# Kernel optimization log

Measured on AMD Instinct MI355X. Metric: run time of the kernel, lower is better.

The kernel has to match this reference:

```python
import jax, jax.numpy as jnp
import numpy as np

N_NODES = 100000
N_EDGES = 1600000
IN_DIM = 128
OUT_DIM = 64
SLOPE = 0.2


def setup_inputs() -> dict:
    key = jax.random.key(0)
    k1, k2, k3, k4 = jax.random.split(key, 4)
    h = jax.random.normal(k1, (N_NODES, IN_DIM), dtype=jnp.float32)
    W = jax.random.normal(k2, (OUT_DIM, IN_DIM), dtype=jnp.float32) * (1.0 / np.sqrt(IN_DIM))
    src = jax.random.randint(k3, (N_EDGES,), 0, N_NODES, dtype=jnp.int64)
    dst = jax.random.randint(k4, (N_EDGES,), 0, N_NODES, dtype=jnp.int64)
    return {"h": h, "W": W, "src": src, "dst": dst}


def reference(h, W, src, dst):
    n = h.shape[0]
    z = h @ W.T                                   # [N, out_dim]
    z_src = z[src]                                # [E, out_dim]
    z_dst = z[dst]                                # [E, out_dim]
    e = jax.nn.leaky_relu(jnp.sum(z_src * z_dst, axis=1), negative_slope=SLOPE)  # [E]
    # segment softmax over incoming edges of each destination node
    m = jax.ops.segment_max(e, dst, num_segments=n)        # [N], -inf for isolated nodes
    ex = jnp.exp(e - m[dst])                                # [E]
    denom = jax.ops.segment_sum(ex, dst, num_segments=n)    # [N]
    alpha = ex / denom[dst]                                 # [E]
    agg = jax.ops.segment_sum(alpha[:, None] * z_src, dst, num_segments=n)  # [N, out_dim]
    return jax.nn.elu(agg)
```

## Files before the change

kernel.cpp:

```cpp
#include <hip/hip_runtime.h>
#include <math.h>

#define SLOPE 0.2f
#define LOG2E 1.4426950408889634f

__global__ __launch_bounds__(256, 8) void gemm_hist_kernel(const float* __restrict__ h,
                                                           const float* __restrict__ W,
                                                           float* __restrict__ z,
                                                           const int* __restrict__ dst,
                                                           int* __restrict__ cnt,
                                                           int* __restrict__ rank,
                                                           int n, int ne, int nbGemm) {
    if ((int)blockIdx.x >= nbGemm) {
        int i = (blockIdx.x - nbGemm) * 256 + threadIdx.x;
        int base = i * 4;
        if (base + 3 < ne) {
            int4 d = *(const int4*)(dst + base);
            int4 r;
            r.x = atomicAdd(&cnt[d.x], 1);
            r.y = atomicAdd(&cnt[d.y], 1);
            r.z = atomicAdd(&cnt[d.z], 1);
            r.w = atomicAdd(&cnt[d.w], 1);
            *(int4*)(rank + base) = r;
        } else if (base < ne) {
            for (int rr = base; rr < ne; rr++) rank[rr] = atomicAdd(&cnt[dst[rr]], 1);
        }
        return;
    }

    __shared__ float ws[128][36];
    int t = threadIdx.x;
    int nblk = blockIdx.x >> 1;
    int ch0  = (blockIdx.x & 1) << 5;
    const float4* __restrict__ W4 = reinterpret_cast<const float4*>(W);
#pragma unroll
    for (int j = 0; j < 4; j++) {
        int idx = t + j * 256;
        int o  = idx >> 5;
        int kq = idx & 31;
        float4 w = W4[(size_t)(ch0 + o) * 32 + kq];
        int k = kq << 2;
        int col = o ^ ((kq & 7) << 2);
        ws[k + 0][col] = w.x; ws[k + 1][col] = w.y;
        ws[k + 2][col] = w.z; ws[k + 3][col] = w.w;
    }
    __syncthreads();

    int ng = t >> 3, og = t & 7;
    int n0 = nblk * 64 + ng * 2;
    if (n0 >= n) return;
    const float* __restrict__ hp = h + (size_t)n0 * 128;

    float acc[2][4] = {};
#pragma unroll 4
    for (int k = 0; k < 128; k += 4) {
        int m = (k >> 2) & 7;
        int colb = (og ^ m) << 2;
        float4 hv[2], wv[4];
#pragma unroll
        for (int i = 0; i < 2; i++) hv[i] = *(const float4*)(hp + i * 128 + k);
#pragma unroll
        for (int kk = 0; kk < 4; kk++) wv[kk] = *(const float4*)&ws[k + kk][colb];
#pragma unroll
        for (int i = 0; i < 2; i++) {
            acc[i][0] += hv[i].x * wv[0].x + hv[i].y * wv[1].x + hv[i].z * wv[2].x + hv[i].w * wv[3].x;
            acc[i][1] += hv[i].x * wv[0].y + hv[i].y * wv[1].y + hv[i].z * wv[2].y + hv[i].w * wv[3].y;
            acc[i][2] += hv[i].x * wv[0].z + hv[i].y * wv[1].z + hv[i].z * wv[2].z + hv[i].w * wv[3].z;
            acc[i][3] += hv[i].x * wv[0].w + hv[i].y * wv[1].w + hv[i].z * wv[2].w + hv[i].w * wv[3].w;
        }
    }
#pragma unroll
    for (int i = 0; i < 2; i++) {
        *(float4*)&z[(size_t)(n0 + i) * 64 + ch0 + og * 4] =
            make_float4(acc[i][0], acc[i][1], acc[i][2], acc[i][3]);
    }
}

__global__ __launch_bounds__(256) void scan1(const int* __restrict__ cnt,
                                             int* __restrict__ starts,
                                             int* __restrict__ bsums, int n) {
    __shared__ int ls[256];
    int tbase = blockIdx.x * 4096 + threadIdx.x * 16;
    int v[16];
    int s = 0;
#pragma unroll
    for (int k = 0; k < 16; k++) {
        int idx = tbase + k;
        int c = idx < n ? cnt[idx] : 0;
        v[k] = c; s += c;
    }
    ls[threadIdx.x] = s;
    __syncthreads();
    for (int off = 1; off < 256; off <<= 1) {
        int t = threadIdx.x >= off ? ls[threadIdx.x - off] : 0;
        __syncthreads();
        ls[threadIdx.x] += t;
        __syncthreads();
    }
    int run = ls[threadIdx.x] - s;
    if (threadIdx.x == 255) bsums[blockIdx.x] = ls[255];
#pragma unroll
    for (int k = 0; k < 16; k++) {
        int idx = tbase + k;
        if (idx < n) starts[idx] = run;
        run += v[k];
    }
}

__global__ __launch_bounds__(256) void scan3(int* __restrict__ starts,
                                             const int* __restrict__ bsums,
                                             int n, int ne) {
    __shared__ int base_s;
    int i = blockIdx.x * 256 + threadIdx.x;
    if (threadIdx.x == 0) {
        int reg = (int)(blockIdx.x >> 4);
        int s = 0;
        for (int b = 0; b < reg; b++) s += bsums[b];
        base_s = s;
        if (blockIdx.x == 0) starts[n] = ne;
    }
    __syncthreads();
    if (i < n) starts[i] += base_s;
}

__global__ __launch_bounds__(256) void scatter8_kernel(const int* __restrict__ src,
                                                       const int* __restrict__ dst,
                                                       const int* __restrict__ starts,
                                                       const int* __restrict__ rank,
                                                       int* __restrict__ csr_src, int ne) {
    int i = blockIdx.x * 256 + threadIdx.x;
    int base = i * 8;
    if (base + 7 < ne) {
        int4 s0 = *(const int4*)(src + base),  s1 = *(const int4*)(src + base + 4);
        int4 d0 = *(const int4*)(dst + base),  d1 = *(const int4*)(dst + base + 4);
        int4 r0 = *(const int4*)(rank + base), r1 = *(const int4*)(rank + base + 4);
        csr_src[starts[d0.x] + r0.x] = s0.x;
        csr_src[starts[d0.y] + r0.y] = s0.y;
        csr_src[starts[d0.z] + r0.z] = s0.z;
        csr_src[starts[d0.w] + r0.w] = s0.w;
        csr_src[starts[d1.x] + r1.x] = s1.x;
        csr_src[starts[d1.y] + r1.y] = s1.y;
        csr_src[starts[d1.z] + r1.z] = s1.z;
        csr_src[starts[d1.w] + r1.w] = s1.w;
    } else {
        for (int r = base; r < ne; r++)
            csr_src[starts[dst[r]] + rank[r]] = src[r];
    }
}

__global__ __launch_bounds__(256) void fused_node(const float4* __restrict__ z4,
                                                  const int* __restrict__ starts,
                                                  const int* __restrict__ csr_src,
                                                  float4* __restrict__ out4, int n) {
    int node = blockIdx.x * 4 + (threadIdx.x >> 6);
    if (node >= n) return;
    int lane = threadIdx.x & 63;
    int g = lane >> 4;
    int q = lane & 15;
    int rs = starts[node], re = starts[node + 1];
    float4 zd = z4[(size_t)node * 16 + q];

    float m2 = -1e30f, denom = 0.f;
    float4 acc = make_float4(0.f, 0.f, 0.f, 0.f);

    for (int c = rs; c < re; c += 64) {
        int j = c + lane;
        int sv = j < re ? csr_src[j] : 0;
        int cn = min(64, re - c);
        bool val0 = g < cn;
        int  s0 = __shfl(sv, val0 ? g : 0);
        float4 v0 = z4[(size_t)s0 * 16 + q];
        bool val1 = 4 + g < cn;
        int  s1 = __shfl(sv, val1 ? 4 + g : 0);
        float4 v1 = z4[(size_t)s1 * 16 + q];
        for (int k = 0; k < cn; k += 4) {
            int idx2 = k + 8 + g;
            bool val2 = idx2 < cn;
            int  s2 = __shfl(sv, val2 ? idx2 : 0);
            float4 v2 = z4[(size_t)s2 * 16 + q];
            float p = v0.x * zd.x + v0.y * zd.y + v0.z * zd.z + v0.w * zd.w;
#pragma unroll
            for (int msk = 1; msk < 16; msk <<= 1) p += __shfl_xor(p, msk);
            float e = p > 0.f ? p : SLOPE * p;
            float e2 = e * LOG2E;
            e2 = val0 ? e2 : -2e30f;
            if (__any(e2 > m2)) {
                float mnew = fmaxf(m2, e2);
                float sc = exp2f(m2 - mnew);
                float ex = exp2f(e2 - mnew);
                denom = fmaf(denom, sc, ex);
                acc.x = fmaf(acc.x, sc, ex * v0.x);
                acc.y = fmaf(acc.y, sc, ex * v0.y);
                acc.z = fmaf(acc.z, sc, ex * v0.z);
                acc.w = fmaf(acc.w, sc, ex * v0.w);
                m2 = mnew;
            } else {
                float ex = exp2f(e2 - m2);
                denom += ex;
                acc.x = fmaf(ex, v0.x, acc.x);
                acc.y = fmaf(ex, v0.y, acc.y);
                acc.z = fmaf(ex, v0.z, acc.z);
                acc.w = fmaf(ex, v0.w, acc.w);
            }
            v0 = v1; val0 = val1;
            v1 = v2; val1 = val2;
        }
    }
#pragma unroll
    for (int msk = 16; msk < 64; msk <<= 1) {
        float mo  = __shfl_xor(m2, msk);
        float dno = __shfl_xor(denom, msk);
        float ax = __shfl_xor(acc.x, msk);
        float ay = __shfl_xor(acc.y, msk);
        float az = __shfl_xor(acc.z, msk);
        float aw = __shfl_xor(acc.w, msk);
        float mnew = fmaxf(m2, mo);
        float ss = exp2f(m2 - mnew), so = exp2f(mo - mnew);
        denom = fmaf(denom, ss, dno * so);
        acc.x = fmaf(acc.x, ss, ax * so);
        acc.y = fmaf(acc.y, ss, ay * so);
        acc.z = fmaf(acc.z, ss, az * so);
        acc.w = fmaf(acc.w, ss, aw * so);
        m2 = mnew;
    }
    if (lane < 16) {
        float inv = denom > 0.f ? 1.f / denom : 0.f;
        float4 r; float x;
        x = acc.x * inv; r.x = x > 0.f ? x : __expf(x) - 1.f;
        x = acc.y * inv; r.y = x > 0.f ? x : __expf(x) - 1.f;
        x = acc.z * inv; r.z = x > 0.f ? x : __expf(x) - 1.f;
        x = acc.w * inv; r.w = x > 0.f ? x : __expf(x) - 1.f;
        out4[(size_t)node * 16 + q] = r;
    }
}

extern "C" void kernel_launch(void* const* d_in, const int* in_sizes, int n_in,
                              void* d_out, int out_size, void* d_ws, size_t ws_size,
                              hipStream_t stream) {
    const float* h   = (const float*)d_in[0];
    const float* W   = (const float*)d_in[1];
    const int*   src = (const int*)d_in[2];
    const int*   dst = (const int*)d_in[3];
    int n  = in_sizes[0] / 128;
    int ne = in_sizes[2];

    float* z       = (float*)d_ws;
    int*   rank    = (int*)(z + (size_t)n * 64);
    int*   csr_src = rank + ne;
    int*   cnt     = csr_src + ne;
    int*   starts  = cnt + n;
    int*   bsums   = starts + ((n + 5) & ~3);

    int nbGemm = ((n + 63) / 64) * 2;
    int nbHist = (ne / 4 + 255) / 256;
    int nb_scan = (n + 4095) / 4096;

    hipMemsetAsync(cnt, 0, (size_t)n * sizeof(int), stream);
    gemm_hist_kernel<<<nbGemm + nbHist, 256, 0, stream>>>(h, W, z, dst, cnt, rank,
                                                          n, ne, nbGemm);
    scan1<<<nb_scan, 256, 0, stream>>>(cnt, starts, bsums, n);
    scan3<<<(n + 255) / 256, 256, 0, stream>>>(starts, bsums, n, ne);
    scatter8_kernel<<<(ne / 8 + 255) / 256, 256, 0, stream>>>(src, dst, starts,
                                                              rank, csr_src, ne);
    fused_node<<<(n + 3) / 4, 256, 0, stream>>>((const float4*)z, starts, csr_src,
                                                (float4*)d_out, n);
}
```

Measured before the change: 207.0 us.

## Privatize histogram into 8 counter copies, pack ranks as 16-bit, interleave GEMM/hist blocks

The destination histogram is split across 8 private counter arrays, chosen by edge chunk, to spread atomic traffic. The scan sums the 8 copies, and scan3 turns each copy into its own exclusive offset base so the scatter can index it directly. Per-edge ranks are stored as 16-bit values to halve that traffic. Histogram blocks are also interleaved 1:2 with GEMM blocks so both kinds of work run together. The cost is 8x larger counter memset and scan reads, plus an implicit assumption that the histogram and GEMM block counts line up and that per-copy ranks fit in 16 bits.

```diff
diff --git a/kernel.cpp b/kernel.cpp
--- a/kernel.cpp
+++ b/kernel.cpp
@@ -8,30 +8,37 @@
                                                            const float* __restrict__ W,
                                                            float* __restrict__ z,
                                                            const int* __restrict__ dst,
-                                                           int* __restrict__ cnt,
-                                                           int* __restrict__ rank,
-                                                           int n, int ne, int nbGemm) {
-    if ((int)blockIdx.x >= nbGemm) {
-        int i = (blockIdx.x - nbGemm) * 256 + threadIdx.x;
+                                                           int* __restrict__ cnt8,
+                                                           unsigned short* __restrict__ rank,
+                                                           int n, int ne) {
+    int g = blockIdx.x / 3;
+    int r = blockIdx.x % 3;
+    if (r == 2) {
+        int* __restrict__ cnt = cnt8 + (size_t)(g & 7) * n;
+        int i = g * 256 + threadIdx.x;
         int base = i * 4;
         if (base + 3 < ne) {
             int4 d = *(const int4*)(dst + base);
-            int4 r;
-            r.x = atomicAdd(&cnt[d.x], 1);
-            r.y = atomicAdd(&cnt[d.y], 1);
-            r.z = atomicAdd(&cnt[d.z], 1);
-            r.w = atomicAdd(&cnt[d.w], 1);
-            *(int4*)(rank + base) = r;
+            unsigned int r0 = atomicAdd(&cnt[d.x], 1);
+            unsigned int r1 = atomicAdd(&cnt[d.y], 1);
+            unsigned int r2 = atomicAdd(&cnt[d.z], 1);
+            unsigned int r3 = atomicAdd(&cnt[d.w], 1);
+            uint2 packed;
+            packed.x = (r1 << 16) | (r0 & 0xFFFF);
+            packed.y = (r3 << 16) | (r2 & 0xFFFF);
+            *(uint2*)(rank + base) = packed;
         } else if (base < ne) {
-            for (int rr = base; rr < ne; rr++) rank[rr] = atomicAdd(&cnt[dst[rr]], 1);
+            for (int rr = base; rr < ne; rr++)
+                rank[rr] = (unsigned short)atomicAdd(&cnt[dst[rr]], 1);
         }
         return;
     }
 
     __shared__ float ws[128][36];
     int t = threadIdx.x;
-    int nblk = blockIdx.x >> 1;
-    int ch0  = (blockIdx.x & 1) << 5;
+    int gemmIdx = 2 * g + r;
+    int nblk = gemmIdx >> 1;
+    int ch0  = (gemmIdx & 1) << 5;
     const float4* __restrict__ W4 = reinterpret_cast<const float4*>(W);
 #pragma unroll
     for (int j = 0; j < 4; j++) {
@@ -76,19 +83,35 @@
     }
 }
 
-__global__ __launch_bounds__(256) void scan1(const int* __restrict__ cnt,
+__global__ __launch_bounds__(256) void scan1(const int* __restrict__ cnt8,
                                              int* __restrict__ starts,
                                              int* __restrict__ bsums, int n) {
     __shared__ int ls[256];
     int tbase = blockIdx.x * 4096 + threadIdx.x * 16;
-    int v[16];
+    int tot[16];
+#pragma unroll
+    for (int k = 0; k < 16; k++) tot[k] = 0;
+    if (tbase + 15 < n) {
+#pragma unroll
+        for (int c = 0; c < 8; c++) {
+            const int* cp = cnt8 + (size_t)c * n + tbase;
+#pragma unroll
+            for (int q = 0; q < 4; q++) {
+                int4 v = *(const int4*)(cp + q * 4);
+                tot[q * 4 + 0] += v.x; tot[q * 4 + 1] += v.y;
+                tot[q * 4 + 2] += v.z; tot[q * 4 + 3] += v.w;
+            }
+        }
+    } else {
+        for (int k = 0; k < 16; k++) {
+            int idx = tbase + k;
+            if (idx < n)
+                for (int c = 0; c < 8; c++) tot[k] += cnt8[(size_t)c * n + idx];
+        }
+    }
     int s = 0;
 #pragma unroll
-    for (int k = 0; k < 16; k++) {
-        int idx = tbase + k;
-        int c = idx < n ? cnt[idx] : 0;
-        v[k] = c; s += c;
-    }
+    for (int k = 0; k < 16; k++) s += tot[k];
     ls[threadIdx.x] = s;
     __syncthreads();
     for (int off = 1; off < 256; off <<= 1) {
@@ -103,12 +126,13 @@
     for (int k = 0; k < 16; k++) {
         int idx = tbase + k;
         if (idx < n) starts[idx] = run;
-        run += v[k];
+        run += tot[k];
     }
 }
 
 __global__ __launch_bounds__(256) void scan3(int* __restrict__ starts,
                                              const int* __restrict__ bsums,
+                                             int* __restrict__ cnt8,
                                              int n, int ne) {
     __shared__ int base_s;
     int i = blockIdx.x * 256 + threadIdx.x;
@@ -120,31 +144,44 @@
         if (blockIdx.x == 0) starts[n] = ne;
     }
     __syncthreads();
-    if (i < n) starts[i] += base_s;
+    if (i >= n) return;
+    int b = starts[i] + base_s;
+    starts[i] = b;
+#pragma unroll
+    for (int c = 0; c < 8; c++) {
+        size_t off = (size_t)c * n + i;
+        int t = cnt8[off];
+        cnt8[off] = b;
+        b += t;
+    }
 }
 
 __global__ __launch_bounds__(256) void scatter8_kernel(const int* __restrict__ src,
                                                        const int* __restrict__ dst,
-                                                       const int* __restrict__ starts,
-                                                       const int* __restrict__ rank,
-                                                       int* __restrict__ csr_src, int ne) {
+                                                       const int* __restrict__ cnt8,
+                                                       const unsigned short* __restrict__ rank,
+                                                       int* __restrict__ csr_src,
+                                                       int n, int ne) {
     int i = blockIdx.x * 256 + threadIdx.x;
     int base = i * 8;
     if (base + 7 < ne) {
+        const int* __restrict__ cb = cnt8 + (size_t)((base >> 10) & 7) * n;
         int4 s0 = *(const int4*)(src + base),  s1 = *(const int4*)(src + base + 4);
         int4 d0 = *(const int4*)(dst + base),  d1 = *(const int4*)(dst + base + 4);
-        int4 r0 = *(const int4*)(rank + base), r1 = *(const int4*)(rank + base + 4);
-        csr_src[starts[d0.x] + r0.x] = s0.x;
-        csr_src[starts[d0.y] + r0.y] = s0.y;
-        csr_src[starts[d0.z] + r0.z] = s0.z;
-        csr_src[starts[d0.w] + r0.w] = s0.w;
-        csr_src[starts[d1.x] + r1.x] = s1.x;
-        csr_src[starts[d1.y] + r1.y] = s1.y;
-        csr_src[starts[d1.z] + r1.z] = s1.z;
-        csr_src[starts[d1.w] + r1.w] = s1.w;
+        uint4 rp = *(const uint4*)(rank + base);
+        csr_src[cb[d0.x] + (rp.x & 0xFFFF)] = s0.x;
+        csr_src[cb[d0.y] + (rp.x >> 16)]    = s0.y;
+        csr_src[cb[d0.z] + (rp.y & 0xFFFF)] = s0.z;
+        csr_src[cb[d0.w] + (rp.y >> 16)]    = s0.w;
+        csr_src[cb[d1.x] + (rp.z & 0xFFFF)] = s1.x;
+        csr_src[cb[d1.y] + (rp.z >> 16)]    = s1.y;
+        csr_src[cb[d1.z] + (rp.w & 0xFFFF)] = s1.z;
+        csr_src[cb[d1.w] + (rp.w >> 16)]    = s1.w;
     } else {
-        for (int r = base; r < ne; r++)
-            csr_src[starts[dst[r]] + rank[r]] = src[r];
+        for (int e = base; e < ne; e++) {
+            const int* cb = cnt8 + (size_t)((e >> 10) & 7) * n;
+            csr_src[cb[dst[e]] + rank[e]] = src[e];
+        }
     }
 }
 
@@ -244,24 +281,23 @@
     int n  = in_sizes[0] / 128;
     int ne = in_sizes[2];
 
-    float* z       = (float*)d_ws;
-    int*   rank    = (int*)(z + (size_t)n * 64);
-    int*   csr_src = rank + ne;
-    int*   cnt     = csr_src + ne;
-    int*   starts  = cnt + n;
-    int*   bsums   = starts + ((n + 5) & ~3);
-
-    int nbGemm = ((n + 63) / 64) * 2;
+    float*          z       = (float*)d_ws;
+    unsigned short* rank    = (unsigned short*)(z + (size_t)n * 64);
+    int*            cnt8    = (int*)(rank + ne);
+    int*            csr_src = cnt8 + (size_t)8 * n;
+    int*            starts  = csr_src + ne;
+    int*            bsums   = starts + ((n + 5) & ~3);
+
     int nbHist = (ne / 4 + 255) / 256;
+    int nbTotal = nbHist * 3;
     int nb_scan = (n + 4095) / 4096;
 
-    hipMemsetAsync(cnt, 0, (size_t)n * sizeof(int), stream);
-    gemm_hist_kernel<<<nbGemm + nbHist, 256, 0, stream>>>(h, W, z, dst, cnt, rank,
-                                                          n, ne, nbGemm);
-    scan1<<<nb_scan, 256, 0, stream>>>(cnt, starts, bsums, n);
-    scan3<<<(n + 255) / 256, 256, 0, stream>>>(starts, bsums, n, ne);
-    scatter8_kernel<<<(ne / 8 + 255) / 256, 256, 0, stream>>>(src, dst, starts,
-                                                              rank, csr_src, ne);
+    hipMemsetAsync(cnt8, 0, (size_t)8 * n * sizeof(int), stream);
+    gemm_hist_kernel<<<nbTotal, 256, 0, stream>>>(h, W, z, dst, cnt8, rank, n, ne);
+    scan1<<<nb_scan, 256, 0, stream>>>(cnt8, starts, bsums, n);
+    scan3<<<(n + 255) / 256, 256, 0, stream>>>(starts, bsums, cnt8, n, ne);
+    scatter8_kernel<<<(ne / 8 + 255) / 256, 256, 0, stream>>>(src, dst, cnt8,
+                                                              rank, csr_src, n, ne);
     fused_node<<<(n + 3) / 4, 256, 0, stream>>>((const float4*)z, starts, csr_src,
                                                 (float4*)d_out, n);
 }
```

After: 196.8 us. 1.05x faster.
